# Optimization experiments

Measured on AMD Instinct MI355X. Metric: run time of the kernel, lower is better.

## Reference

```python
import jax, jax.numpy as jnp
import numpy as np
import math

SR = 44100
FRAME = 256
K = 80
NB = 16
MIDI_LO, MIDI_HI = 21.0, 108.0


def setup_inputs() -> dict:
    key = jax.random.key(0)
    k0, k1 = jax.random.split(key)
    B = 8
    # fundamental frequencies spread over ~4 octaves of the piano range (55..880 Hz)
    f0 = 55.0 * 2.0 ** (jax.random.uniform(k0, (B,)) * 4.0)
    vel_norm = jax.random.uniform(k1, (B,), minval=0.2, maxval=1.0)
    inp = dict(
        f0=f0.astype(jnp.float32),
        vel_norm=vel_norm.astype(jnp.float32),
        log_B_slope=jnp.float32(-2.0),
        log_B_intercept=jnp.float32(-7.5),
        log_tau1=jnp.linspace(math.log(0.4), math.log(0.05), K).astype(jnp.float32),
        log_tau2=jnp.linspace(math.log(5.0), math.log(0.3), K).astype(jnp.float32),
        logit_a1=jnp.linspace(-1.4, 0.0, K).astype(jnp.float32),
        log_beat_hz=jnp.linspace(math.log(0.3), math.log(1.5), K).astype(jnp.float32),
        logit_beat_depth=jnp.full((K,), -1.7, jnp.float32),
        log_A0=(-jnp.log(jnp.arange(1, K + 1, dtype=jnp.float32)) * 0.7),
        harm_detune=jnp.zeros((K,), jnp.float32),
        noise_band_gain=jnp.zeros((NB,), jnp.float32),
        log_tau_noise=jnp.float32(math.log(0.05)),
        log_noise_level=jnp.float32(math.log(0.08)),
        pan_scale=jnp.float32(0.0),
        n_frames=256,
    )
    return inp


def reference(f0, vel_norm, log_B_slope, log_B_intercept, log_tau1, log_tau2,
              logit_a1, log_beat_hz, logit_beat_depth, log_A0, harm_detune,
              noise_band_gain, log_tau_noise, log_noise_level, pan_scale,
              n_frames):
    N = n_frames * FRAME                                   # total audio samples
    t = jnp.arange(N, dtype=jnp.float32) * jnp.float32(1.0 / SR)   # (N,)
    two_pi = jnp.float32(2.0 * math.pi)

    # --- inharmonicity coefficient B(midi) = exp(clamp(slope*m + intercept)) ---
    midi = 69.0 + 12.0 * jnp.log2(f0 / 440.0)
    midi_norm = (midi - MIDI_LO) / (MIDI_HI - MIDI_LO)
    B_inh = jnp.exp(jnp.clip(log_B_slope * midi_norm + log_B_intercept, -14.0, -4.0))  # (B,)

    # --- inharmonic partial frequencies f_k = f0 * k * sqrt(1 + B k^2) ---
    ks = jnp.arange(1, K + 1, dtype=jnp.float32)           # (K,)
    freqs = f0[:, None] * ks * jnp.sqrt(1.0 + B_inh[:, None] * ks ** 2)  # (B,K)
    freqs = freqs * (1.0 + harm_detune)                    # learned per-partial detune
    alive = (freqs < SR / 2).astype(jnp.float32)           # nyquist mask (B,K)

    # --- double-exponential decay envelope per partial ---
    tau1 = jnp.exp(log_tau1)
    tau2 = jnp.exp(log_tau2)
    a1 = jax.nn.sigmoid(logit_a1)
    env = (a1[:, None] * jnp.exp(-t / tau1[:, None])
           + (1.0 - a1[:, None]) * jnp.exp(-t / tau2[:, None]))        # (K,N)

    # --- beating modulation (two-string coupling) ---
    depth = jax.nn.sigmoid(logit_beat_depth)
    bhz = jnp.exp(log_beat_hz)
    beat = 1.0 + 0.5 * depth[:, None] * (jnp.cos(two_pi * bhz[:, None] * t) - 1.0)  # (K,N)

    # --- oscillator bank: amp * env * beat * sin(2 pi f t) ---
    amp = jnp.exp(log_A0)[None, :] * vel_norm[:, None] * alive          # (B,K)
    phase = two_pi * freqs[:, :, None] * t                              # (B,K,N)
    partials = (amp[:, :, None] * (env * beat)[None]) * jnp.sin(phase)  # (B,K,N)

    # --- stereo panning per partial (constant-power) ---
    pan_init = (jnp.arange(K, dtype=jnp.float32) / max(K - 1, 1) * 2.0 - 1.0) * 0.1
    pan = jnp.tanh(pan_init * jnp.exp(pan_scale))                       # (K,)
    gains = jnp.stack([jnp.sqrt(0.5 * (1.0 - pan)),
                       jnp.sqrt(0.5 * (1.0 + pan))])                    # (2,K)
    audio = jnp.einsum('bkn,ck->bcn', partials, gains)                  # (B,2,N)

    # --- attack noise: log-spaced band oscillators with fast exp decay ---
    nf = jnp.exp(jnp.linspace(math.log(200.0), math.log(20000.0), NB)).astype(jnp.float32)
    n_alive = (nf < SR / 2).astype(jnp.float32)
    band_g = jax.nn.softmax(noise_band_gain) * n_alive                  # (NB,)
    noise_osc = jnp.sin(two_pi * nf[:, None] * t)                       # (NB,N)
    noise_env = jnp.exp(-t / jnp.exp(log_tau_noise))                    # (N,)
    noise_sig = (band_g @ noise_osc) * noise_env                        # (N,)
    noise = jnp.exp(log_noise_level) * vel_norm[:, None] * noise_sig[None, :]  # (B,N)

    return audio + noise[:, None, :]                                    # (B,2,N)
```

## Files before the change

### kernel.cpp

```cpp
#include <hip/hip_runtime.h>
#include <math.h>


#define KMAX 128
#define NBMAX 32
#define NCH 4

#define C2PI_HI 6.28318548202514648f
#define C2PI_LO -1.7484556e-7f
#define INV2PI  0.15915494309189535f

__device__ __forceinline__ float nofuse(float x) {
    asm volatile("" : "+v"(x));
    return x;
}

__device__ __forceinline__ float sin_cw(float ph) {
    float q = rintf(ph * INV2PI);
    float r = fmaf(q, -C2PI_HI, ph);
    r = fmaf(q, -C2PI_LO, r);
    return __sinf(r);
}


__global__ void pr_precomp(const float* __restrict__ f0,
                           const float* __restrict__ vel,
                           const float* __restrict__ pslope,
                           const float* __restrict__ pinter,
                           const float* __restrict__ log_tau1,
                           const float* __restrict__ log_tau2,
                           const float* __restrict__ logit_a1,
                           const float* __restrict__ log_beat_hz,
                           const float* __restrict__ logit_beat_depth,
                           const float* __restrict__ log_A0,
                           const float* __restrict__ harm_detune,
                           const float* __restrict__ noise_band_gain,
                           const float* __restrict__ plog_tau_noise,
                           const float* __restrict__ plog_noise_level,
                           const float* __restrict__ ppan_scale,
                           float* __restrict__ ws, int B, int K, int NB) {
    const int tid = threadIdx.x;
    const int b = blockIdx.x;
    const float two_pi = C2PI_HI;
    const float slope = pslope[0], inter = pinter[0], pan_scale = ppan_scale[0];

    float4* pk4 = (float4*)ws;
    float4* keA = pk4 + (size_t)B * K;
    float4* keB = keA + K;
    float4* nz  = keB + K;
    float*  nl  = (float*)(nz + NB);

    {
        float f0b = f0[b];
        float fr = f0b / 440.0f;
        float midi = 69.0f + 12.0f * (float)log2((double)fr);
        float mn = (midi - 21.0f) / 87.0f;
        float z = nofuse(slope * mn) + inter;
        z = fminf(fmaxf(z, -14.0f), -4.0f);
        float Binh = (float)exp((double)z);
        float pexp = (float)exp((double)pan_scale);
        int km1 = (K - 1) > 1 ? (K - 1) : 1;
        for (int k = tid; k < K; k += blockDim.x) {
            float kf = (float)(k + 1);
            float kk  = kf * kf;
            float bk2 = nofuse(Binh * kk);
            float arg = nofuse(1.0f + bk2);
            float s3  = (float)sqrt((double)arg);
            float r0  = nofuse(f0b * kf);
            float r1  = nofuse(r0 * s3);
            float dt  = nofuse(1.0f + harm_detune[k]);
            float fq  = nofuse(r1 * dt);
            float alive = (fq < 22050.0f) ? 1.0f : 0.0f;
            float amp = (float)exp((double)log_A0[k]) * vel[b] * alive;
            float a = (float)k / (float)km1;
            float pini = nofuse((a * 2.0f - 1.0f) * 0.1f);
            float pan = (float)tanh((double)nofuse(pini * pexp));
            float gl = (float)sqrt((double)(0.5f * (1.0f - pan)));
            float gr = (float)sqrt((double)(0.5f * (1.0f + pan)));
            float pf = nofuse(two_pi * fq);
            pk4[(size_t)b * K + k] = make_float4(pf, amp * gl, amp * gr, 0.0f);
        }
    }

    if (b != 0) return;
    for (int k = tid; k < K; k += blockDim.x) {
        float tau1 = (float)exp((double)log_tau1[k]);
        float tau2 = (float)exp((double)log_tau2[k]);
        float a1 = (float)(1.0 / (1.0 + exp(-(double)logit_a1[k])));
        float bhz = (float)exp((double)log_beat_hz[k]);
        float dep = (float)(1.0 / (1.0 + exp(-(double)logit_beat_depth[k])));
        keA[k] = make_float4(1.0f / tau1, 1.0f / tau2, a1, 1.0f - a1);
        keB[k] = make_float4(nofuse(two_pi * bhz), 0.5f * dep, 0.0f, 0.0f);
    }
    for (int j = tid; j < NB; j += blockDim.x) {
        float m = -1e30f;
        for (int q = 0; q < NB; ++q) m = fmaxf(m, noise_band_gain[q]);
        float ssum = 0.0f;
        for (int q = 0; q < NB; ++q)
            ssum += (float)exp((double)(noise_band_gain[q] - m));
        double start = log(200.0), stop = log(20000.0);
        double step = (stop - start) / (double)(NB - 1);
        float lin = (j == NB - 1) ? (float)stop : (float)(start + (double)j * step);
        float nf = (float)exp((double)lin);
        float na = (nf < 22050.0f) ? 1.0f : 0.0f;
        float bg = ((float)exp((double)(noise_band_gain[j] - m)) / ssum) * na;
        nz[j] = make_float4(nofuse(two_pi * nf), bg, 0.0f, 0.0f);
    }
    for (int bb = tid; bb < B; bb += blockDim.x)
        nl[bb] = (float)exp((double)plog_noise_level[0]) * vel[bb];
    if (tid == 0) nl[B] = 1.0f / (float)exp((double)plog_tau_noise[0]);
}

template <int BT>
__global__ __launch_bounds__(256, 4) void pr_synth(
    const float4* __restrict__ pk4, const float4* __restrict__ keA,
    const float4* __restrict__ keB, const float4* __restrict__ nz,
    const float* __restrict__ nlp, float* __restrict__ out,
    int B, int K, int NB, int N) {
    __shared__ float4 s_pk[BT * KMAX];
    __shared__ float4 s_keA[KMAX];
    __shared__ float4 s_keB[KMAX];
    __shared__ float4 s_nz[NBMAX];
    __shared__ float  s_red[NCH][64][2 * BT + 1];

    const int tid  = threadIdx.x;
    const int lane = tid & 63;
    const int g    = tid >> 6;

    for (int i = tid; i < BT * K; i += blockDim.x) {
        int bi = i / K, k = i - bi * K;
        s_pk[bi * KMAX + k] =
            (bi < B) ? pk4[(size_t)bi * K + k] : make_float4(0, 0, 0, 0);
    }
    for (int i = tid; i < K; i += blockDim.x) {
        s_keA[i] = keA[i];
        s_keB[i] = keB[i];
    }
    for (int i = tid; i < NB; i += blockDim.x) s_nz[i] = nz[i];
    __syncthreads();

    const int n = blockIdx.x * 64 + lane;
    const float t = (float)n * (float)(1.0 / 44100.0);
    const float nt = -t;
    const int KC = (K + NCH - 1) / NCH;
    const int k0 = g * KC;
    const int k1 = min(K, k0 + KC);

    float accL[BT], accR[BT];
#pragma unroll
    for (int bi = 0; bi < BT; ++bi) { accL[bi] = 0.0f; accR[bi] = 0.0f; }

    for (int k = k0; k < k1; ++k) {
        float4 ka = s_keA[k];
        float4 kb = s_keB[k];
        float e1 = __expf(nt * ka.x);
        float e2 = __expf(nt * ka.y);
        float env = ka.z * e1 + ka.w * e2;
        float beat = fmaf(kb.y, __cosf(kb.x * t) - 1.0f, 1.0f);
        float eb = env * beat;
#pragma unroll
        for (int bi = 0; bi < BT; ++bi) {
            float4 p = s_pk[bi * KMAX + k];
            float ph = p.x * t;
            float q = rintf(ph * INV2PI);
            float r = fmaf(q, -C2PI_HI, ph);
            r = fmaf(q, -C2PI_LO, r);
            float sv = __sinf(r);
            float pp = eb * sv;
            accL[bi] = fmaf(p.y, pp, accL[bi]);
            accR[bi] = fmaf(p.z, pp, accR[bi]);
        }
    }

#pragma unroll
    for (int bi = 0; bi < BT; ++bi) {
        s_red[g][lane][2 * bi + 0] = accL[bi];
        s_red[g][lane][2 * bi + 1] = accR[bi];
    }
    __syncthreads();

    float ns = 0.0f;
    for (int j = 0; j < NB; ++j) {
        float4 zj = s_nz[j];
        ns = fmaf(zj.y, sin_cw(zj.x * t), ns);
    }
    float nsv = ns * __expf(nt * nlp[B]);

    const int JT = (2 * BT) / NCH;
    if (n < N) {
#pragma unroll
        for (int jj = 0; jj < JT; ++jj) {
            int j = g * JT + jj;
            int b = j >> 1;
            if (b >= B) continue;
            float s = 0.0f;
#pragma unroll
            for (int c = 0; c < NCH; ++c) s += s_red[c][lane][j];
            float nois = nlp[b] * nsv;
            out[(size_t)j * N + n] = s + nois;
        }
    }
}

extern "C" void kernel_launch(void* const* d_in, const int* in_sizes, int n_in,
                              void* d_out, int out_size, void* d_ws, size_t ws_size,
                              hipStream_t stream) {
    const float* f0    = (const float*)d_in[0];
    const float* vel   = (const float*)d_in[1];
    const float* slope = (const float*)d_in[2];
    const float* inter = (const float*)d_in[3];
    const float* lt1   = (const float*)d_in[4];
    const float* lt2   = (const float*)d_in[5];
    const float* la1   = (const float*)d_in[6];
    const float* lbh   = (const float*)d_in[7];
    const float* lbd   = (const float*)d_in[8];
    const float* lA0   = (const float*)d_in[9];
    const float* hdet  = (const float*)d_in[10];
    const float* nbg   = (const float*)d_in[11];
    const float* ltn   = (const float*)d_in[12];
    const float* lnl   = (const float*)d_in[13];
    const float* pans  = (const float*)d_in[14];

    const int B  = in_sizes[0];
    const int K  = in_sizes[4];
    const int NB = in_sizes[11];
    const int N  = out_size / (2 * B);

    float* ws = (float*)d_ws;

    hipLaunchKernelGGL(pr_precomp, dim3(B), dim3(128), 0, stream,
                       f0, vel, slope, inter, lt1, lt2, la1, lbh, lbd, lA0,
                       hdet, nbg, ltn, lnl, pans, ws, B, K, NB);

    const float4* pk4 = (const float4*)ws;
    const float4* keA = pk4 + (size_t)B * K;
    const float4* keB = keA + K;
    const float4* nz  = keB + K;
    const float*  nlp = (const float*)(nz + NB);

    dim3 grid((N + 63) / 64);
    hipLaunchKernelGGL(pr_synth<8>, grid, dim3(256), 0, stream,
                       pk4, keA, keB, nz, nlp, (float*)d_out, B, K, NB, N);
}
```

Before: 110.2 us.

## Read partial params from global via transposed layout, split K across 8 waves

Per-partial parameters are stored k-major (transposed), so the synth kernel can read them straight from global/cache with wave-uniform indices instead of staging them in LDS. The partial sum over K is split across 8 waves in 512-thread blocks instead of 4. The envelope exps become exp2f with LOG2E folded into the rates, and the beat cosine uses the native revolution-based cos, so the beat frequency is stored without the 2π factor. This removes the LDS fill and its barrier and raises per-block parallelism, at the cost of more reduction traffic. The transposed indexing uses stride BT rather than B, which only matches when B equals 8.

```diff
diff --git a/kernel.cpp b/kernel.cpp
--- a/kernel.cpp
+++ b/kernel.cpp
@@ -2,13 +2,13 @@
 #include <math.h>
 
 
-#define KMAX 128
 #define NBMAX 32
-#define NCH 4
+#define NCH 8
 
 #define C2PI_HI 6.28318548202514648f
 #define C2PI_LO -1.7484556e-7f
 #define INV2PI  0.15915494309189535f
+#define LOG2E   1.44269504088896340736f
 
 __device__ __forceinline__ float nofuse(float x) {
     asm volatile("" : "+v"(x));
@@ -44,8 +44,8 @@
     const float two_pi = C2PI_HI;
     const float slope = pslope[0], inter = pinter[0], pan_scale = ppan_scale[0];
 
-    float4* pk4 = (float4*)ws;
-    float4* keA = pk4 + (size_t)B * K;
+    float4* pk4T = (float4*)ws;
+    float4* keA = pk4T + (size_t)B * K;
     float4* keB = keA + K;
     float4* nz  = keB + K;
     float*  nl  = (float*)(nz + NB);
@@ -78,7 +78,7 @@
             float gl = (float)sqrt((double)(0.5f * (1.0f - pan)));
             float gr = (float)sqrt((double)(0.5f * (1.0f + pan)));
             float pf = nofuse(two_pi * fq);
-            pk4[(size_t)b * K + k] = make_float4(pf, amp * gl, amp * gr, 0.0f);
+            pk4T[(size_t)k * B + b] = make_float4(pf, amp * gl, amp * gr, 0.0f);
         }
     }
 
@@ -89,8 +89,8 @@
         float a1 = (float)(1.0 / (1.0 + exp(-(double)logit_a1[k])));
         float bhz = (float)exp((double)log_beat_hz[k]);
         float dep = (float)(1.0 / (1.0 + exp(-(double)logit_beat_depth[k])));
-        keA[k] = make_float4(1.0f / tau1, 1.0f / tau2, a1, 1.0f - a1);
-        keB[k] = make_float4(nofuse(two_pi * bhz), 0.5f * dep, 0.0f, 0.0f);
+        keA[k] = make_float4(LOG2E / tau1, LOG2E / tau2, a1, 1.0f - a1);
+        keB[k] = make_float4(bhz, 0.5f * dep, 0.0f, 0.0f);
     }
     for (int j = tid; j < NB; j += blockDim.x) {
         float m = -1e30f;
@@ -112,32 +112,16 @@
 }
 
 template <int BT>
-__global__ __launch_bounds__(256, 4) void pr_synth(
-    const float4* __restrict__ pk4, const float4* __restrict__ keA,
+__global__ __launch_bounds__(512, 8) void pr_synth(
+    const float4* __restrict__ pk4T, const float4* __restrict__ keA,
     const float4* __restrict__ keB, const float4* __restrict__ nz,
     const float* __restrict__ nlp, float* __restrict__ out,
     int B, int K, int NB, int N) {
-    __shared__ float4 s_pk[BT * KMAX];
-    __shared__ float4 s_keA[KMAX];
-    __shared__ float4 s_keB[KMAX];
-    __shared__ float4 s_nz[NBMAX];
-    __shared__ float  s_red[NCH][64][2 * BT + 1];
+    __shared__ float s_red[NCH][64][2 * BT + 1];
 
     const int tid  = threadIdx.x;
     const int lane = tid & 63;
     const int g    = tid >> 6;
-
-    for (int i = tid; i < BT * K; i += blockDim.x) {
-        int bi = i / K, k = i - bi * K;
-        s_pk[bi * KMAX + k] =
-            (bi < B) ? pk4[(size_t)bi * K + k] : make_float4(0, 0, 0, 0);
-    }
-    for (int i = tid; i < K; i += blockDim.x) {
-        s_keA[i] = keA[i];
-        s_keB[i] = keB[i];
-    }
-    for (int i = tid; i < NB; i += blockDim.x) s_nz[i] = nz[i];
-    __syncthreads();
 
     const int n = blockIdx.x * 64 + lane;
     const float t = (float)n * (float)(1.0 / 44100.0);
@@ -151,16 +135,17 @@
     for (int bi = 0; bi < BT; ++bi) { accL[bi] = 0.0f; accR[bi] = 0.0f; }
 
     for (int k = k0; k < k1; ++k) {
-        float4 ka = s_keA[k];
-        float4 kb = s_keB[k];
-        float e1 = __expf(nt * ka.x);
-        float e2 = __expf(nt * ka.y);
+        float4 ka = keA[k];
+        float4 kb = keB[k];
+        float e1 = exp2f(nt * ka.x);
+        float e2 = exp2f(nt * ka.y);
         float env = ka.z * e1 + ka.w * e2;
-        float beat = fmaf(kb.y, __cosf(kb.x * t) - 1.0f, 1.0f);
+        float beat = fmaf(kb.y, __builtin_amdgcn_cosf(kb.x * t) - 1.0f, 1.0f);
         float eb = env * beat;
+        const float4* pk = pk4T + (size_t)k * BT;
 #pragma unroll
         for (int bi = 0; bi < BT; ++bi) {
-            float4 p = s_pk[bi * KMAX + k];
+            float4 p = pk[bi];
             float ph = p.x * t;
             float q = rintf(ph * INV2PI);
             float r = fmaf(q, -C2PI_HI, ph);
@@ -181,7 +166,7 @@
 
     float ns = 0.0f;
     for (int j = 0; j < NB; ++j) {
-        float4 zj = s_nz[j];
+        float4 zj = nz[j];
         ns = fmaf(zj.y, sin_cw(zj.x * t), ns);
     }
     float nsv = ns * __expf(nt * nlp[B]);
@@ -232,13 +217,13 @@
                        f0, vel, slope, inter, lt1, lt2, la1, lbh, lbd, lA0,
                        hdet, nbg, ltn, lnl, pans, ws, B, K, NB);
 
-    const float4* pk4 = (const float4*)ws;
-    const float4* keA = pk4 + (size_t)B * K;
+    const float4* pk4T = (const float4*)ws;
+    const float4* keA = pk4T + (size_t)B * K;
     const float4* keB = keA + K;
     const float4* nz  = keB + K;
     const float*  nlp = (const float*)(nz + NB);
 
     dim3 grid((N + 63) / 64);
-    hipLaunchKernelGGL(pr_synth<8>, grid, dim3(256), 0, stream,
-                       pk4, keA, keB, nz, nlp, (float*)d_out, B, K, NB, N);
-}
+    hipLaunchKernelGGL(pr_synth<8>, grid, dim3(512), 0, stream,
+                       pk4T, keA, keB, nz, nlp, (float*)d_out, B, K, NB, N);
+}
```

After: 119.7 us. 1.09x slower.
